# Optimization experiments

Measured on AMD Instinct MI355X. Metric: run time of the kernel, lower is better.

The kernel has to match this reference:

```python
import jax, jax.numpy as jnp
import numpy as np

D_MODEL = 1024
NHEADS = 16
E_HEAD = D_MODEL // NHEADS  # 64
ROPE_BASE = 10000.0


def _rope_cos_sin(L, dim, base, dtype):
    # dim = E_head (even); inv_freq over pairs, GPT-NeoX half-split convention
    inv_freq = 1.0 / (base ** (jnp.arange(0, dim, 2, dtype=jnp.float32) / dim))
    pos = jnp.arange(L, dtype=jnp.float32)
    freqs = pos[:, None] * inv_freq[None, :]  # [L, dim/2]
    return jnp.cos(freqs).astype(dtype), jnp.sin(freqs).astype(dtype)


def _apply_rope(t, cos, sin):
    # t: [B, H, L, Dh]; rotate-half formulation
    d2 = t.shape[-1] // 2
    t1, t2 = t[..., :d2], t[..., d2:]
    return jnp.concatenate([t1 * cos - t2 * sin, t1 * sin + t2 * cos], axis=-1)


def setup_inputs() -> dict:
    key = jax.random.key(0)
    ks = jax.random.split(key, 5)
    B, L = 4, 2048
    x = jax.random.normal(ks[0], (B, L, D_MODEL), dtype=jnp.float32)
    s_in = 1.0 / np.sqrt(D_MODEL)
    W_packed = jax.random.normal(ks[1], (3 * D_MODEL, D_MODEL), dtype=jnp.float32) * s_in
    b_packed = jax.random.normal(ks[2], (3 * D_MODEL,), dtype=jnp.float32) * 0.02
    W_out = jax.random.normal(ks[3], (D_MODEL, D_MODEL), dtype=jnp.float32) * s_in
    b_out = jax.random.normal(ks[4], (D_MODEL,), dtype=jnp.float32) * 0.02
    return {"x": x, "W_packed": W_packed, "b_packed": b_packed, "W_out": W_out, "b_out": b_out}


def reference(x, W_packed, b_packed, W_out, b_out):
    B, L, _ = x.shape
    # 1) packed QKV projection (query is key is value path)
    qkv = jnp.einsum('ble,fe->blf', x, W_packed) + b_packed  # [B, L, 3*D]
    q, k, v = jnp.split(qkv, 3, axis=-1)
    # 2) split heads -> [B, H, L, Dh]
    def heads(t):
        return t.reshape(B, L, NHEADS, E_HEAD).transpose(0, 2, 1, 3)
    q, k, v = heads(q), heads(k), heads(v)
    # 3) RoPE on q, k
    cos, sin = _rope_cos_sin(L, E_HEAD, ROPE_BASE, x.dtype)
    q = _apply_rope(q, cos, sin)
    k = _apply_rope(k, cos, sin)
    # 4) SDPA (non-causal, no dropout)
    scale = 1.0 / np.sqrt(E_HEAD)
    scores = jnp.einsum('bhqd,bhkd->bhqk', q, k) * scale
    attn = jax.nn.softmax(scores, axis=-1)
    out = jnp.einsum('bhqk,bhkd->bhqd', attn, v)
    # 5) merge heads + output projection
    out = out.transpose(0, 2, 1, 3).reshape(B, L, D_MODEL)
    return jnp.einsum('bld,ed->ble', out, W_out) + b_out
```

## Files before the change

kernel.cpp:

```cpp
#include <hip/hip_runtime.h>
#include <hip/hip_bf16.h>
#include <stdint.h>

#define L_SEQ 2048
#define NB    4
#define NH    16
#define EH    64
#define DM    1024
#define MTOT  (NB * L_SEQ)

typedef __attribute__((ext_vector_type(8))) short bf16x8;
typedef __attribute__((ext_vector_type(4))) float f32x4;
typedef __attribute__((ext_vector_type(16))) float f32x16;
typedef __attribute__((ext_vector_type(2))) unsigned uint2v;

static __device__ __forceinline__ float bf2f(short u) {
    union { unsigned int i; float f; } c;
    c.i = ((unsigned int)(unsigned short)u) << 16;
    return c.f;
}
static __device__ __forceinline__ short f2bf(float f) {
    union { float f; unsigned int i; } c; c.f = f;
    unsigned int x = c.i;
    unsigned int r = (x + 0x7fffu + ((x >> 16) & 1u)) >> 16;
    return (short)(unsigned short)r;
}
static __device__ __forceinline__ unsigned cvtpk(float lo, float hi) {
    unsigned r;
    asm volatile("v_cvt_pk_bf16_f32 %0, %1, %2" : "=v"(r) : "v"(lo), "v"(hi));
    return r;
}
static __device__ __forceinline__ float pairmax(float x) {
    union { float f; unsigned u; } c; c.f = x;
    uint2v r = __builtin_amdgcn_permlane32_swap(c.u, c.u, false, false);
    union { unsigned u; float f; } a, b; a.u = r[0]; b.u = r[1];
    return fmaxf(a.f, b.f);
}
static __device__ __forceinline__ float pairsum(float x) {
    union { float f; unsigned u; } c; c.f = x;
    uint2v r = __builtin_amdgcn_permlane32_swap(c.u, c.u, false, false);
    union { unsigned u; float f; } a, b; a.u = r[0]; b.u = r[1];
    return a.f + b.f;
}

static __device__ __forceinline__ void gload_lds16(const void* g, void* lds) {
    __builtin_amdgcn_global_load_lds(
        (const __attribute__((address_space(1))) unsigned int*)g,
        (__attribute__((address_space(3))) unsigned int*)lds, 16, 0, 0);
}

__global__ __launch_bounds__(256) void cvt_k(const float* __restrict__ in,
                                             short* __restrict__ out, int n4) {
    int i = blockIdx.x * 256 + threadIdx.x;
    if (i >= n4) return;
    float4 v = ((const float4*)in)[i];
    short4 o;
    o.x = f2bf(v.x); o.y = f2bf(v.y); o.z = f2bf(v.z); o.w = f2bf(v.w);
    ((short4*)out)[i] = o;
}

__global__ __launch_bounds__(256) void rope_table_k(float* __restrict__ tab) {
    int i = blockIdx.x * 256 + threadIdx.x;
    int l = i >> 5, d = i & 31;
    float inv = powf(10000.0f, -(float)d * (1.0f / 32.0f));
    float fr = (float)l * inv;
    tab[i]         = cosf(fr);
    tab[65536 + i] = sinf(fr);
}

template<int OUTBF16>
__global__ __launch_bounds__(256) void gemm_bt_k(const short* __restrict__ A,
                                                 const short* __restrict__ Bt,
                                                 const float* __restrict__ bias,
                                                 void* __restrict__ Cv,
                                                 int N, int K) {
    __shared__ short As[128 * 64];
    __shared__ short Bs[128 * 64];
    const int t = threadIdx.x;
    const int w = t >> 6, l = t & 63;
    const int wr = w >> 1, wc = w & 1;
    const int lr = l & 15, lh = l >> 4;
    const int m0 = blockIdx.y * 128, n0 = blockIdx.x * 128;
    const int srow = t >> 3;
    const int scol = (t & 7) * 8;

    f32x4 acc[4][4] = {};

    const short* Ab = A + (size_t)(m0 + srow) * K + scol;
    const short* Bb = Bt + (size_t)(n0 + srow) * K + scol;

    for (int k0 = 0; k0 < K; k0 += 64) {
        __syncthreads();
#pragma unroll
        for (int i = 0; i < 4; i++) {
            gload_lds16(Ab + (size_t)(i * 32) * K + k0, As + i * 2048 + w * 512);
            gload_lds16(Bb + (size_t)(i * 32) * K + k0, Bs + i * 2048 + w * 512);
        }
        __syncthreads();
#pragma unroll
        for (int kk = 0; kk < 2; kk++) {
            bf16x8 af[4], bfr[4];
#pragma unroll
            for (int mi = 0; mi < 4; mi++)
                af[mi] = *(const bf16x8*)(As + (wr * 64 + mi * 16 + lr) * 64 + kk * 32 + lh * 8);
#pragma unroll
            for (int nj = 0; nj < 4; nj++)
                bfr[nj] = *(const bf16x8*)(Bs + (wc * 64 + nj * 16 + lr) * 64 + kk * 32 + lh * 8);
            __builtin_amdgcn_s_setprio(1);
#pragma unroll
            for (int mi = 0; mi < 4; mi++)
#pragma unroll
                for (int nj = 0; nj < 4; nj++)
                    acc[mi][nj] = __builtin_amdgcn_mfma_f32_16x16x32_bf16(
                        af[mi], bfr[nj], acc[mi][nj], 0, 0, 0);
            __builtin_amdgcn_s_setprio(0);
        }
    }
#pragma unroll
    for (int mi = 0; mi < 4; mi++) {
#pragma unroll
        for (int nj = 0; nj < 4; nj++) {
            const int row = m0 + wr * 64 + mi * 16 + lh * 4;
            const int col = n0 + wc * 64 + nj * 16 + lr;
            const float bsv = bias[col];
#pragma unroll
            for (int j = 0; j < 4; j++) {
                float v = acc[mi][nj][j] + bsv;
                if (OUTBF16)
                    ((short*)Cv)[(size_t)(row + j) * N + col] = f2bf(v);
                else
                    ((float*)Cv)[(size_t)(row + j) * N + col] = v;
            }
        }
    }
}

__global__ __launch_bounds__(256) void rope_scatter_k(const short* __restrict__ qkv,
                                                      const float* __restrict__ tab,
                                                      short* __restrict__ Q,
                                                      short* __restrict__ Kd) {
    int idx = blockIdx.x * 256 + threadIdx.x;
    int d = idx & 31;
    int h = (idx >> 5) & 15;
    int bl = idx >> 9;
    int l = bl & (L_SEQ - 1);
    int b = bl >> 11;
    float c = tab[l * 32 + d], s = tab[65536 + l * 32 + d];
    const short* row = qkv + (size_t)bl * 3072;
    float q1 = bf2f(row[h * 64 + d]);
    float q2 = bf2f(row[h * 64 + d + 32]);
    float k1 = bf2f(row[1024 + h * 64 + d]);
    float k2 = bf2f(row[1024 + h * 64 + d + 32]);
    size_t ob = ((size_t)((b * 16 + h) * 2048 + l)) * 64;
    const float sc = 0.18033688011112042f;
    Q[ob + d]       = f2bf((q1 * c - q2 * s) * sc);
    Q[ob + d + 32]  = f2bf((q1 * s + q2 * c) * sc);
    int r7 = l & 7;
    int c1 = ((d >> 3) ^ r7) * 8 + (d & 7);
    int c2 = (((d >> 3) | 4) ^ r7) * 8 + (d & 7);
    Kd[ob + c1] = f2bf(k1 * c - k2 * s);
    Kd[ob + c2] = f2bf(k1 * s + k2 * c);
}

__global__ __launch_bounds__(256) void v_trans_k(const short* __restrict__ qkv,
                                                 short* __restrict__ Vt) {
    __shared__ short tile[64 * 65];
    int bh = blockIdx.y;
    int l0 = blockIdx.x * 64;
    int t = threadIdx.x;
    int b = bh >> 4, h = bh & 15;
#pragma unroll
    for (int i = 0; i < 16; i++) {
        int l = i * 4 + (t >> 6);
        int d = t & 63;
        tile[d * 65 + l] = qkv[(size_t)(b * 2048 + l0 + l) * 3072 + 2048 + h * 64 + d];
    }
    __syncthreads();
#pragma unroll
    for (int i = 0; i < 16; i++) {
        int d = i * 4 + (t >> 6);
        int lx = t & 63;
        int cl = (lx & ~0xC) | ((lx & 4) << 1) | ((lx & 8) >> 1);
        int lp = l0 | ((((cl >> 3) ^ (d & 7)) << 3)) | (cl & 7);
        Vt[(size_t)(bh * 64 + d) * 2048 + lp] = tile[d * 65 + lx];
    }
}

__global__ __launch_bounds__(512, 4) void attn_k(const short* __restrict__ Qg,
                                                 const short* __restrict__ Kg,
                                                 const short* __restrict__ Vt,
                                                 short* __restrict__ O) {
    __shared__ short Ks[2][64 * 64];
    __shared__ short Vs[2][64 * 64];
    const int t = threadIdx.x;
    const int w = t >> 6, l = t & 63;
    const int q = l & 31, hi = l >> 5;
    const int r7 = l & 7;

    const int od = blockIdx.x + blockIdx.y * 8;
    const int qblk = (od >> 3) & 7;
    const int bh = (od & 7) * 8 + (od >> 6);
    const int q0 = qblk * 256;

    const short* Qb = Qg + (size_t)bh * (2048 * 64);
    const short* Kb = Kg + (size_t)bh * (2048 * 64);
    const short* Vb = Vt + (size_t)bh * (64 * 2048);

    const int qrow = q0 + w * 32 + q;
    bf16x8 qf[4];
#pragma unroll
    for (int ds = 0; ds < 4; ds++)
        qf[ds] = *(const bf16x8*)(Qb + (size_t)qrow * 64 + ds * 16 + hi * 8);

    f32x16 o0 = {}, o1 = {};
    float m = -1e30f, lsum = 0.0f;

    const int grow = w * 8 + (l >> 3);
    const int gcol = r7 * 8;

    gload_lds16(Kb + (size_t)grow * 64 + gcol, &Ks[0][w * 512]);
    gload_lds16(Vb + (size_t)grow * 2048 + gcol, &Vs[0][w * 512]);
    __syncthreads();

    for (int it = 0; it < 32; ++it) {
        const int cur = it & 1;
        const short* Kc = &Ks[cur][0];
        const short* Vc = &Vs[cur][0];
        if (it < 31) {
            const int kn = (it + 1) * 64;
            gload_lds16(Kb + (size_t)(kn + grow) * 64 + gcol, &Ks[cur ^ 1][w * 512]);
            gload_lds16(Vb + (size_t)grow * 2048 + kn + gcol, &Vs[cur ^ 1][w * 512]);
        }

        f32x16 s0 = {}, s1 = {};
#pragma unroll
        for (int ds = 0; ds < 4; ds++) {
            const int ch = ((ds << 1) | hi) ^ r7;
            bf16x8 k0f = *(const bf16x8*)(Kc + q * 64 + ch * 8);
            bf16x8 k1f = *(const bf16x8*)(Kc + (32 + q) * 64 + ch * 8);
            __builtin_amdgcn_s_setprio(1);
            s0 = __builtin_amdgcn_mfma_f32_32x32x16_bf16(k0f, qf[ds], s0, 0, 0, 0);
            s1 = __builtin_amdgcn_mfma_f32_32x32x16_bf16(k1f, qf[ds], s1, 0, 0, 0);
            __builtin_amdgcn_s_setprio(0);
        }

        float tm[16];
#pragma unroll
        for (int r = 0; r < 16; r++) tm[r] = fmaxf(s0[r], s1[r]);
#pragma unroll
        for (int st = 8; st >= 1; st >>= 1)
#pragma unroll
            for (int i = 0; i < 8; i++) if (i < st) tm[i] = fmaxf(tm[i], tm[i + st]);
        float pm = pairmax(tm[0]);

        if (__any((int)(pm > m + 8.0f))) {
            float mn = fmaxf(m, pm);
            float sc = __builtin_amdgcn_exp2f(m - mn);
            lsum *= sc;
#pragma unroll
            for (int r = 0; r < 16; r++) { o0[r] *= sc; o1[r] *= sc; }
            m = mn;
        }

#pragma unroll
        for (int r = 0; r < 16; r++) {
            s0[r] = __builtin_amdgcn_exp2f(s0[r] - m);
            s1[r] = __builtin_amdgcn_exp2f(s1[r] - m);
        }
        float ts[16];
#pragma unroll
        for (int r = 0; r < 16; r++) ts[r] = s0[r] + s1[r];
#pragma unroll
        for (int st = 8; st >= 1; st >>= 1)
#pragma unroll
            for (int i = 0; i < 8; i++) if (i < st) ts[i] = ts[i] + ts[i + st];
        lsum += pairsum(ts[0]);

        bf16x8 pf[4];
        {
            union { unsigned u[4]; bf16x8 v; } f;
            f.u[0] = cvtpk(s0[0], s0[1]);  f.u[1] = cvtpk(s0[2], s0[3]);
            f.u[2] = cvtpk(s0[4], s0[5]);  f.u[3] = cvtpk(s0[6], s0[7]);
            pf[0] = f.v;
            f.u[0] = cvtpk(s0[8], s0[9]);  f.u[1] = cvtpk(s0[10], s0[11]);
            f.u[2] = cvtpk(s0[12], s0[13]); f.u[3] = cvtpk(s0[14], s0[15]);
            pf[1] = f.v;
            f.u[0] = cvtpk(s1[0], s1[1]);  f.u[1] = cvtpk(s1[2], s1[3]);
            f.u[2] = cvtpk(s1[4], s1[5]);  f.u[3] = cvtpk(s1[6], s1[7]);
            pf[2] = f.v;
            f.u[0] = cvtpk(s1[8], s1[9]);  f.u[1] = cvtpk(s1[10], s1[11]);
            f.u[2] = cvtpk(s1[12], s1[13]); f.u[3] = cvtpk(s1[14], s1[15]);
            pf[3] = f.v;
        }

#pragma unroll
        for (int ks = 0; ks < 4; ks++) {
            const int ch = ((ks << 1) | hi) ^ r7;
            bf16x8 v0f = *(const bf16x8*)(Vc + q * 64 + ch * 8);
            bf16x8 v1f = *(const bf16x8*)(Vc + (32 + q) * 64 + ch * 8);
            __builtin_amdgcn_s_setprio(1);
            o0 = __builtin_amdgcn_mfma_f32_32x32x16_bf16(v0f, pf[ks], o0, 0, 0, 0);
            o1 = __builtin_amdgcn_mfma_f32_32x32x16_bf16(v1f, pf[ks], o1, 0, 0, 0);
            __builtin_amdgcn_s_setprio(0);
        }

        __syncthreads();
    }

    const float inv = 1.0f / lsum;
    const int b = bh >> 4, h = bh & 15;
    short* Orow = O + (size_t)(b * 2048 + qrow) * 1024 + h * 64;
#pragma unroll
    for (int g = 0; g < 4; g++) {
        unsigned w0 = cvtpk(o0[g * 4 + 0] * inv, o0[g * 4 + 1] * inv);
        unsigned w1 = cvtpk(o0[g * 4 + 2] * inv, o0[g * 4 + 3] * inv);
        unsigned long long p0 = (unsigned long long)w0 | ((unsigned long long)w1 << 32);
        *(unsigned long long*)(Orow + g * 8 + hi * 4) = p0;
        unsigned w2 = cvtpk(o1[g * 4 + 0] * inv, o1[g * 4 + 1] * inv);
        unsigned w3 = cvtpk(o1[g * 4 + 2] * inv, o1[g * 4 + 3] * inv);
        unsigned long long p1 = (unsigned long long)w2 | ((unsigned long long)w3 << 32);
        *(unsigned long long*)(Orow + 32 + g * 8 + hi * 4) = p1;
    }
}

extern "C" void kernel_launch(void* const* d_in, const int* in_sizes, int n_in,
                              void* d_out, int out_size, void* d_ws, size_t ws_size,
                              hipStream_t stream) {
    const float* x  = (const float*)d_in[0];
    const float* Wp = (const float*)d_in[1];
    const float* bp = (const float*)d_in[2];
    const float* Wo = (const float*)d_in[3];
    const float* bo = (const float*)d_in[4];

    char* ws = (char*)d_ws;
    const size_t SZ_XB  = (size_t)MTOT * DM * 2;
    const size_t SZ_WPB = (size_t)3 * DM * DM * 2;
    const size_t SZ_WOB = (size_t)DM * DM * 2;
    const size_t SZ_QKV = (size_t)MTOT * 3 * DM * 2;
    const size_t SZ_BHLE = (size_t)MTOT * DM * 2;

    short* xb   = (short*)(ws);
    short* wpb  = (short*)(ws + SZ_XB);
    short* wob  = (short*)(ws + SZ_XB + SZ_WPB);
    short* qkvb = (short*)(ws + SZ_XB + SZ_WPB + SZ_WOB);
    short* Qb   = (short*)(ws + SZ_XB + SZ_WPB + SZ_WOB + SZ_QKV);
    short* Kb   = (short*)(ws + SZ_XB + SZ_WPB + SZ_WOB + SZ_QKV + SZ_BHLE);
    short* Vtb  = (short*)(ws + SZ_XB + SZ_WPB + SZ_WOB + SZ_QKV + 2 * SZ_BHLE);
    short* Ob   = (short*)(ws + SZ_XB + SZ_WPB + SZ_WOB + SZ_QKV + 3 * SZ_BHLE);
    float* tab  = (float*)(ws + SZ_XB + SZ_WPB + SZ_WOB + SZ_QKV + 4 * SZ_BHLE);

    cvt_k<<<8192, 256, 0, stream>>>(x, xb, MTOT * DM / 4);
    cvt_k<<<3072, 256, 0, stream>>>(Wp, wpb, 3 * DM * DM / 4);
    cvt_k<<<1024, 256, 0, stream>>>(Wo, wob, DM * DM / 4);
    rope_table_k<<<256, 256, 0, stream>>>(tab);

    gemm_bt_k<1><<<dim3(24, 64), 256, 0, stream>>>(xb, wpb, bp, qkvb, 3 * DM, DM);

    rope_scatter_k<<<16384, 256, 0, stream>>>(qkvb, tab, Qb, Kb);
    v_trans_k<<<dim3(32, 64), 256, 0, stream>>>(qkvb, Vtb);

    attn_k<<<dim3(8, 64), 512, 0, stream>>>(Qb, Kb, Vtb, Ob);

    gemm_bt_k<0><<<dim3(8, 64), 256, 0, stream>>>(Ob, wob, bo, d_out, DM, DM);
}
```

Before: 220.3 us.

## Fuse RoPE and V transpose into QKV GEMM epilogue, merge casts, MFMA row sums

The QKV GEMM now applies bias, RoPE and scaling itself and writes Q, swizzled K and transposed V straight from its accumulators. This removes the bf16 qkv intermediate and the separate rope_scatter and v_trans kernels. The three fp32-to-bf16 conversion launches are merged into one kernel. In attention, the softmax row sum comes from an extra MFMA against a ones vector instead of shuffle reductions, which adds MFMA work but removes VALU reductions. The new epilogue uses scattered 2-byte stores and per-element table lookups, which may be less coalesced than before.

```diff
diff --git a/kernel.cpp b/kernel.cpp
--- a/kernel.cpp
+++ b/kernel.cpp
@@ -36,12 +36,6 @@
     union { unsigned u; float f; } a, b; a.u = r[0]; b.u = r[1];
     return fmaxf(a.f, b.f);
 }
-static __device__ __forceinline__ float pairsum(float x) {
-    union { float f; unsigned u; } c; c.f = x;
-    uint2v r = __builtin_amdgcn_permlane32_swap(c.u, c.u, false, false);
-    union { unsigned u; float f; } a, b; a.u = r[0]; b.u = r[1];
-    return a.f + b.f;
-}
 
 static __device__ __forceinline__ void gload_lds16(const void* g, void* lds) {
     __builtin_amdgcn_global_load_lds(
@@ -49,14 +43,21 @@
         (__attribute__((address_space(3))) unsigned int*)lds, 16, 0, 0);
 }
 
-__global__ __launch_bounds__(256) void cvt_k(const float* __restrict__ in,
-                                             short* __restrict__ out, int n4) {
-    int i = blockIdx.x * 256 + threadIdx.x;
-    if (i >= n4) return;
-    float4 v = ((const float4*)in)[i];
+__global__ __launch_bounds__(256) void cvt3_k(const float* __restrict__ x,
+                                              const float* __restrict__ wp,
+                                              const float* __restrict__ wo,
+                                              short* __restrict__ xb,
+                                              short* __restrict__ wpb,
+                                              short* __restrict__ wob) {
+    int bid = blockIdx.x;
+    const float* src; short* dst; int i;
+    if (bid < 8192)       { src = x;  dst = xb;  i = bid * 256 + threadIdx.x; }
+    else if (bid < 11264) { src = wp; dst = wpb; i = (bid - 8192) * 256 + threadIdx.x; }
+    else                  { src = wo; dst = wob; i = (bid - 11264) * 256 + threadIdx.x; }
+    float4 v = ((const float4*)src)[i];
     short4 o;
     o.x = f2bf(v.x); o.y = f2bf(v.y); o.z = f2bf(v.z); o.w = f2bf(v.w);
-    ((short4*)out)[i] = o;
+    ((short4*)dst)[i] = o;
 }
 
 __global__ __launch_bounds__(256) void rope_table_k(float* __restrict__ tab) {
@@ -68,12 +69,13 @@
     tab[65536 + i] = sinf(fr);
 }
 
-template<int OUTBF16>
-__global__ __launch_bounds__(256) void gemm_bt_k(const short* __restrict__ A,
-                                                 const short* __restrict__ Bt,
-                                                 const float* __restrict__ bias,
-                                                 void* __restrict__ Cv,
-                                                 int N, int K) {
+__global__ __launch_bounds__(256) void qkv_gemm_k(const short* __restrict__ A,
+                                                  const short* __restrict__ Bt,
+                                                  const float* __restrict__ bias,
+                                                  const float* __restrict__ tab,
+                                                  short* __restrict__ Q,
+                                                  short* __restrict__ Kd,
+                                                  short* __restrict__ Vt) {
     __shared__ short As[128 * 64];
     __shared__ short Bs[128 * 64];
     const int t = threadIdx.x;
@@ -86,15 +88,15 @@
 
     f32x4 acc[4][4] = {};
 
-    const short* Ab = A + (size_t)(m0 + srow) * K + scol;
-    const short* Bb = Bt + (size_t)(n0 + srow) * K + scol;
-
-    for (int k0 = 0; k0 < K; k0 += 64) {
+    const short* Ab = A + (size_t)(m0 + srow) * 1024 + scol;
+    const short* Bb = Bt + (size_t)(n0 + srow) * 1024 + scol;
+
+    for (int k0 = 0; k0 < 1024; k0 += 64) {
         __syncthreads();
 #pragma unroll
         for (int i = 0; i < 4; i++) {
-            gload_lds16(Ab + (size_t)(i * 32) * K + k0, As + i * 2048 + w * 512);
-            gload_lds16(Bb + (size_t)(i * 32) * K + k0, Bs + i * 2048 + w * 512);
+            gload_lds16(Ab + (size_t)(i * 32) * 1024 + k0, As + i * 2048 + w * 512);
+            gload_lds16(Bb + (size_t)(i * 32) * 1024 + k0, Bs + i * 2048 + w * 512);
         }
         __syncthreads();
 #pragma unroll
@@ -116,6 +118,108 @@
             __builtin_amdgcn_s_setprio(0);
         }
     }
+
+    const int part = n0 >> 10;
+    const int h = ((n0 & 1023) >> 6) + wc;
+    const float sc = 0.18033688011112042f;
+
+    if (part == 2) {
+#pragma unroll
+        for (int mi = 0; mi < 4; mi++) {
+            const int rowb = m0 + wr * 64 + mi * 16 + lh * 4;
+            const int b = rowb >> 11;
+            const int lbase = (rowb & 2047) & ~63;
+            const int lp = (((mi * 2 + (lh & 1)) ^ (lr & 7)) << 3) | ((lh >> 1) * 4);
+#pragma unroll
+            for (int nj = 0; nj < 4; nj++) {
+                const int dv = nj * 16 + lr;
+                const float bv = bias[n0 + wc * 64 + nj * 16 + lr];
+                short4 sv;
+                sv.x = f2bf(acc[mi][nj][0] + bv);
+                sv.y = f2bf(acc[mi][nj][1] + bv);
+                sv.z = f2bf(acc[mi][nj][2] + bv);
+                sv.w = f2bf(acc[mi][nj][3] + bv);
+                *(short4*)(Vt + (size_t)((b * 16 + h) * 64 + dv) * 2048 + lbase + lp) = sv;
+            }
+        }
+    } else {
+#pragma unroll
+        for (int mi = 0; mi < 4; mi++) {
+            const int rowb = m0 + wr * 64 + mi * 16 + lh * 4;
+#pragma unroll
+            for (int njl = 0; njl < 2; njl++) {
+                const int d2 = njl * 16 + lr;
+                const float b1 = bias[n0 + wc * 64 + njl * 16 + lr];
+                const float b2 = bias[n0 + wc * 64 + (njl + 2) * 16 + lr];
+#pragma unroll
+                for (int j = 0; j < 4; j++) {
+                    const int rr = rowb + j;
+                    const int ll = rr & 2047, b = rr >> 11;
+                    const float c = tab[ll * 32 + d2], s = tab[65536 + ll * 32 + d2];
+                    const float t1 = acc[mi][njl][j] + b1;
+                    const float t2 = acc[mi][njl + 2][j] + b2;
+                    const size_t ob = ((size_t)((b * 16 + h) * 2048 + ll)) * 64;
+                    if (part == 0) {
+                        Q[ob + d2]      = f2bf((t1 * c - t2 * s) * sc);
+                        Q[ob + d2 + 32] = f2bf((t1 * s + t2 * c) * sc);
+                    } else {
+                        const int r7l = ll & 7;
+                        Kd[ob + (((d2 >> 3) ^ r7l) * 8) + (d2 & 7)]         = f2bf(t1 * c - t2 * s);
+                        Kd[ob + ((((d2 >> 3) | 4) ^ r7l) * 8) + (d2 & 7)]   = f2bf(t1 * s + t2 * c);
+                    }
+                }
+            }
+        }
+    }
+}
+
+__global__ __launch_bounds__(256) void gemm_out_k(const short* __restrict__ A,
+                                                  const short* __restrict__ Bt,
+                                                  const float* __restrict__ bias,
+                                                  float* __restrict__ Cv,
+                                                  int N, int K) {
+    __shared__ short As[128 * 64];
+    __shared__ short Bs[128 * 64];
+    const int t = threadIdx.x;
+    const int w = t >> 6, l = t & 63;
+    const int wr = w >> 1, wc = w & 1;
+    const int lr = l & 15, lh = l >> 4;
+    const int m0 = blockIdx.y * 128, n0 = blockIdx.x * 128;
+    const int srow = t >> 3;
+    const int scol = (t & 7) * 8;
+
+    f32x4 acc[4][4] = {};
+
+    const short* Ab = A + (size_t)(m0 + srow) * K + scol;
+    const short* Bb = Bt + (size_t)(n0 + srow) * K + scol;
+
+    for (int k0 = 0; k0 < K; k0 += 64) {
+        __syncthreads();
+#pragma unroll
+        for (int i = 0; i < 4; i++) {
+            gload_lds16(Ab + (size_t)(i * 32) * K + k0, As + i * 2048 + w * 512);
+            gload_lds16(Bb + (size_t)(i * 32) * K + k0, Bs + i * 2048 + w * 512);
+        }
+        __syncthreads();
+#pragma unroll
+        for (int kk = 0; kk < 2; kk++) {
+            bf16x8 af[4], bfr[4];
+#pragma unroll
+            for (int mi = 0; mi < 4; mi++)
+                af[mi] = *(const bf16x8*)(As + (wr * 64 + mi * 16 + lr) * 64 + kk * 32 + lh * 8);
+#pragma unroll
+            for (int nj = 0; nj < 4; nj++)
+                bfr[nj] = *(const bf16x8*)(Bs + (wc * 64 + nj * 16 + lr) * 64 + kk * 32 + lh * 8);
+            __builtin_amdgcn_s_setprio(1);
+#pragma unroll
+            for (int mi = 0; mi < 4; mi++)
+#pragma unroll
+                for (int nj = 0; nj < 4; nj++)
+                    acc[mi][nj] = __builtin_amdgcn_mfma_f32_16x16x32_bf16(
+                        af[mi], bfr[nj], acc[mi][nj], 0, 0, 0);
+            __builtin_amdgcn_s_setprio(0);
+        }
+    }
 #pragma unroll
     for (int mi = 0; mi < 4; mi++) {
 #pragma unroll
@@ -124,65 +228,9 @@
             const int col = n0 + wc * 64 + nj * 16 + lr;
             const float bsv = bias[col];
 #pragma unroll
-            for (int j = 0; j < 4; j++) {
-                float v = acc[mi][nj][j] + bsv;
-                if (OUTBF16)
-                    ((short*)Cv)[(size_t)(row + j) * N + col] = f2bf(v);
-                else
-                    ((float*)Cv)[(size_t)(row + j) * N + col] = v;
-            }
-        }
-    }
-}
-
-__global__ __launch_bounds__(256) void rope_scatter_k(const short* __restrict__ qkv,
-                                                      const float* __restrict__ tab,
-                                                      short* __restrict__ Q,
-                                                      short* __restrict__ Kd) {
-    int idx = blockIdx.x * 256 + threadIdx.x;
-    int d = idx & 31;
-    int h = (idx >> 5) & 15;
-    int bl = idx >> 9;
-    int l = bl & (L_SEQ - 1);
-    int b = bl >> 11;
-    float c = tab[l * 32 + d], s = tab[65536 + l * 32 + d];
-    const short* row = qkv + (size_t)bl * 3072;
-    float q1 = bf2f(row[h * 64 + d]);
-    float q2 = bf2f(row[h * 64 + d + 32]);
-    float k1 = bf2f(row[1024 + h * 64 + d]);
-    float k2 = bf2f(row[1024 + h * 64 + d + 32]);
-    size_t ob = ((size_t)((b * 16 + h) * 2048 + l)) * 64;
-    const float sc = 0.18033688011112042f;
-    Q[ob + d]       = f2bf((q1 * c - q2 * s) * sc);
-    Q[ob + d + 32]  = f2bf((q1 * s + q2 * c) * sc);
-    int r7 = l & 7;
-    int c1 = ((d >> 3) ^ r7) * 8 + (d & 7);
-    int c2 = (((d >> 3) | 4) ^ r7) * 8 + (d & 7);
-    Kd[ob + c1] = f2bf(k1 * c - k2 * s);
-    Kd[ob + c2] = f2bf(k1 * s + k2 * c);
-}
-
-__global__ __launch_bounds__(256) void v_trans_k(const short* __restrict__ qkv,
-                                                 short* __restrict__ Vt) {
-    __shared__ short tile[64 * 65];
-    int bh = blockIdx.y;
-    int l0 = blockIdx.x * 64;
-    int t = threadIdx.x;
-    int b = bh >> 4, h = bh & 15;
-#pragma unroll
-    for (int i = 0; i < 16; i++) {
-        int l = i * 4 + (t >> 6);
-        int d = t & 63;
-        tile[d * 65 + l] = qkv[(size_t)(b * 2048 + l0 + l) * 3072 + 2048 + h * 64 + d];
-    }
-    __syncthreads();
-#pragma unroll
-    for (int i = 0; i < 16; i++) {
-        int d = i * 4 + (t >> 6);
-        int lx = t & 63;
-        int cl = (lx & ~0xC) | ((lx & 4) << 1) | ((lx & 8) >> 1);
-        int lp = l0 | ((((cl >> 3) ^ (d & 7)) << 3)) | (cl & 7);
-        Vt[(size_t)(bh * 64 + d) * 2048 + lp] = tile[d * 65 + lx];
+            for (int j = 0; j < 4; j++)
+                Cv[(size_t)(row + j) * N + col] = acc[mi][nj][j] + bsv;
+        }
     }
 }
 
@@ -212,8 +260,11 @@
     for (int ds = 0; ds < 4; ds++)
         qf[ds] = *(const bf16x8*)(Qb + (size_t)qrow * 64 + ds * 16 + hi * 8);
 
-    f32x16 o0 = {}, o1 = {};
-    float m = -1e30f, lsum = 0.0f;
+    const short one_bf = (short)0x3F80;
+    const bf16x8 ones = {one_bf, one_bf, one_bf, one_bf, one_bf, one_bf, one_bf, one_bf};
+
+    f32x16 o0 = {}, o1 = {}, os = {};
+    float m = -1e30f;
 
     const int grow = w * 8 + (l >> 3);
     const int gcol = r7 * 8;
@@ -244,21 +295,19 @@
             __builtin_amdgcn_s_setprio(0);
         }
 
-        float tm[16];
-#pragma unroll
-        for (int r = 0; r < 16; r++) tm[r] = fmaxf(s0[r], s1[r]);
-#pragma unroll
-        for (int st = 8; st >= 1; st >>= 1)
-#pragma unroll
-            for (int i = 0; i < 8; i++) if (i < st) tm[i] = fmaxf(tm[i], tm[i + st]);
-        float pm = pairmax(tm[0]);
+        float a[8];
+#pragma unroll
+        for (int i = 0; i < 8; i++)
+            a[i] = fmaxf(fmaxf(s0[i], s0[i + 8]), fmaxf(s1[i], s1[i + 8]));
+        float pm = pairmax(fmaxf(
+            fmaxf(fmaxf(a[0], a[1]), fmaxf(a[2], a[3])),
+            fmaxf(fmaxf(a[4], a[5]), fmaxf(a[6], a[7]))));
 
         if (__any((int)(pm > m + 8.0f))) {
             float mn = fmaxf(m, pm);
             float sc = __builtin_amdgcn_exp2f(m - mn);
-            lsum *= sc;
-#pragma unroll
-            for (int r = 0; r < 16; r++) { o0[r] *= sc; o1[r] *= sc; }
+#pragma unroll
+            for (int r = 0; r < 16; r++) { o0[r] *= sc; o1[r] *= sc; os[r] *= sc; }
             m = mn;
         }
 
@@ -267,14 +316,6 @@
             s0[r] = __builtin_amdgcn_exp2f(s0[r] - m);
             s1[r] = __builtin_amdgcn_exp2f(s1[r] - m);
         }
-        float ts[16];
-#pragma unroll
-        for (int r = 0; r < 16; r++) ts[r] = s0[r] + s1[r];
-#pragma unroll
-        for (int st = 8; st >= 1; st >>= 1)
-#pragma unroll
-            for (int i = 0; i < 8; i++) if (i < st) ts[i] = ts[i] + ts[i + st];
-        lsum += pairsum(ts[0]);
 
         bf16x8 pf[4];
         {
@@ -301,13 +342,14 @@
             __builtin_amdgcn_s_setprio(1);
             o0 = __builtin_amdgcn_mfma_f32_32x32x16_bf16(v0f, pf[ks], o0, 0, 0, 0);
             o1 = __builtin_amdgcn_mfma_f32_32x32x16_bf16(v1f, pf[ks], o1, 0, 0, 0);
+            os = __builtin_amdgcn_mfma_f32_32x32x16_bf16(ones, pf[ks], os, 0, 0, 0);
             __builtin_amdgcn_s_setprio(0);
         }
 
         __syncthreads();
     }
 
-    const float inv = 1.0f / lsum;
+    const float inv = 1.0f / os[0];
     const int b = bh >> 4, h = bh & 15;
     short* Orow = O + (size_t)(b * 2048 + qrow) * 1024 + h * 64;
 #pragma unroll
@@ -336,30 +378,23 @@
     const size_t SZ_XB  = (size_t)MTOT * DM * 2;
     const size_t SZ_WPB = (size_t)3 * DM * DM * 2;
     const size_t SZ_WOB = (size_t)DM * DM * 2;
-    const size_t SZ_QKV = (size_t)MTOT * 3 * DM * 2;
     const size_t SZ_BHLE = (size_t)MTOT * DM * 2;
 
     short* xb   = (short*)(ws);
     short* wpb  = (short*)(ws + SZ_XB);
     short* wob  = (short*)(ws + SZ_XB + SZ_WPB);
-    short* qkvb = (short*)(ws + SZ_XB + SZ_WPB + SZ_WOB);
-    short* Qb   = (short*)(ws + SZ_XB + SZ_WPB + SZ_WOB + SZ_QKV);
-    short* Kb   = (short*)(ws + SZ_XB + SZ_WPB + SZ_WOB + SZ_QKV + SZ_BHLE);
-    short* Vtb  = (short*)(ws + SZ_XB + SZ_WPB + SZ_WOB + SZ_QKV + 2 * SZ_BHLE);
-    short* Ob   = (short*)(ws + SZ_XB + SZ_WPB + SZ_WOB + SZ_QKV + 3 * SZ_BHLE);
-    float* tab  = (float*)(ws + SZ_XB + SZ_WPB + SZ_WOB + SZ_QKV + 4 * SZ_BHLE);
-
-    cvt_k<<<8192, 256, 0, stream>>>(x, xb, MTOT * DM / 4);
-    cvt_k<<<3072, 256, 0, stream>>>(Wp, wpb, 3 * DM * DM / 4);
-    cvt_k<<<1024, 256, 0, stream>>>(Wo, wob, DM * DM / 4);
+    short* Qb   = (short*)(ws + SZ_XB + SZ_WPB + SZ_WOB);
+    short* Kb   = (short*)(ws + SZ_XB + SZ_WPB + SZ_WOB + SZ_BHLE);
+    short* Vtb  = (short*)(ws + SZ_XB + SZ_WPB + SZ_WOB + 2 * SZ_BHLE);
+    short* Ob   = (short*)(ws + SZ_XB + SZ_WPB + SZ_WOB + 3 * SZ_BHLE);
+    float* tab  = (float*)(ws + SZ_XB + SZ_WPB + SZ_WOB + 4 * SZ_BHLE);
+
+    cvt3_k<<<12288, 256, 0, stream>>>(x, Wp, Wo, xb, wpb, wob);
     rope_table_k<<<256, 256, 0, stream>>>(tab);
 
-    gemm_bt_k<1><<<dim3(24, 64), 256, 0, stream>>>(xb, wpb, bp, qkvb, 3 * DM, DM);
-
-    rope_scatter_k<<<16384, 256, 0, stream>>>(qkvb, tab, Qb, Kb);
-    v_trans_k<<<dim3(32, 64), 256, 0, stream>>>(qkvb, Vtb);
+    qkv_gemm_k<<<dim3(24, 64), 256, 0, stream>>>(xb, wpb, bp, tab, Qb, Kb, Vtb);
 
     attn_k<<<dim3(8, 64), 512, 0, stream>>>(Qb, Kb, Vtb, Ob);
 
-    gemm_bt_k<0><<<dim3(8, 64), 256, 0, stream>>>(Ob, wob, bo, d_out, DM, DM);
-}
+    gemm_out_k<<<dim3(8, 64), 256, 0, stream>>>(Ob, wob, bo, (float*)d_out, DM, DM);
+}
```

Result: slower. 229.0 us (+4.0%).

## Use 256x256 double-buffered GEMM, fuse conversions, compute softmax sum via MFMA

Applied to the files above, without the earlier changes.

Replaces the 128x128 single-buffered GEMM with a 512-thread 256x256 tile kernel that uses two-stage LDS prefetch, a swizzled LDS layout and block-index swizzling. The three fp32-to-bf16 conversion launches become one kernel. In attention, the softmax denominator is accumulated by an extra MFMA against a ones vector instead of VALU reductions and lane swaps, and the max reduction is flattened. Larger tiles raise data reuse but yield only 128 blocks for the output projection, which may underfill the GPU; the extra MFMA adds matrix-core work.

```diff
diff --git a/kernel.cpp b/kernel.cpp
--- a/kernel.cpp
+++ b/kernel.cpp
@@ -36,12 +36,6 @@
     union { unsigned u; float f; } a, b; a.u = r[0]; b.u = r[1];
     return fmaxf(a.f, b.f);
 }
-static __device__ __forceinline__ float pairsum(float x) {
-    union { float f; unsigned u; } c; c.f = x;
-    uint2v r = __builtin_amdgcn_permlane32_swap(c.u, c.u, false, false);
-    union { unsigned u; float f; } a, b; a.u = r[0]; b.u = r[1];
-    return a.f + b.f;
-}
 
 static __device__ __forceinline__ void gload_lds16(const void* g, void* lds) {
     __builtin_amdgcn_global_load_lds(
@@ -49,14 +43,21 @@
         (__attribute__((address_space(3))) unsigned int*)lds, 16, 0, 0);
 }
 
-__global__ __launch_bounds__(256) void cvt_k(const float* __restrict__ in,
-                                             short* __restrict__ out, int n4) {
-    int i = blockIdx.x * 256 + threadIdx.x;
-    if (i >= n4) return;
-    float4 v = ((const float4*)in)[i];
+__global__ __launch_bounds__(256) void cvt3_k(const float* __restrict__ x,
+                                              const float* __restrict__ wp,
+                                              const float* __restrict__ wo,
+                                              short* __restrict__ xb,
+                                              short* __restrict__ wpb,
+                                              short* __restrict__ wob) {
+    int bid = blockIdx.x;
+    const float* src; short* dst; int i;
+    if (bid < 8192)       { src = x;  dst = xb;  i = bid * 256 + threadIdx.x; }
+    else if (bid < 11264) { src = wp; dst = wpb; i = (bid - 8192) * 256 + threadIdx.x; }
+    else                  { src = wo; dst = wob; i = (bid - 11264) * 256 + threadIdx.x; }
+    float4 v = ((const float4*)src)[i];
     short4 o;
     o.x = f2bf(v.x); o.y = f2bf(v.y); o.z = f2bf(v.z); o.w = f2bf(v.w);
-    ((short4*)out)[i] = o;
+    ((short4*)dst)[i] = o;
 }
 
 __global__ __launch_bounds__(256) void rope_table_k(float* __restrict__ tab) {
@@ -68,63 +69,91 @@
     tab[65536 + i] = sinf(fr);
 }
 
-template<int OUTBF16>
-__global__ __launch_bounds__(256) void gemm_bt_k(const short* __restrict__ A,
-                                                 const short* __restrict__ Bt,
-                                                 const float* __restrict__ bias,
-                                                 void* __restrict__ Cv,
-                                                 int N, int K) {
-    __shared__ short As[128 * 64];
-    __shared__ short Bs[128 * 64];
+template<int OUTBF16, int NBX>
+__global__ __launch_bounds__(512, 2) void gemm256_k(const short* __restrict__ A,
+                                                    const short* __restrict__ Bt,
+                                                    const float* __restrict__ bias,
+                                                    void* __restrict__ Cv) {
+    __shared__ short lds[2][2][256 * 32];
     const int t = threadIdx.x;
     const int w = t >> 6, l = t & 63;
-    const int wr = w >> 1, wc = w & 1;
+    const int wm = w >> 2, wn = w & 3;
     const int lr = l & 15, lh = l >> 4;
-    const int m0 = blockIdx.y * 128, n0 = blockIdx.x * 128;
-    const int srow = t >> 3;
-    const int scol = (t & 7) * 8;
-
-    f32x4 acc[4][4] = {};
-
-    const short* Ab = A + (size_t)(m0 + srow) * K + scol;
-    const short* Bb = Bt + (size_t)(n0 + srow) * K + scol;
-
-    for (int k0 = 0; k0 < K; k0 += 64) {
-        __syncthreads();
-#pragma unroll
-        for (int i = 0; i < 4; i++) {
-            gload_lds16(Ab + (size_t)(i * 32) * K + k0, As + i * 2048 + w * 512);
-            gload_lds16(Bb + (size_t)(i * 32) * K + k0, Bs + i * 2048 + w * 512);
-        }
-        __syncthreads();
-#pragma unroll
-        for (int kk = 0; kk < 2; kk++) {
-            bf16x8 af[4], bfr[4];
-#pragma unroll
-            for (int mi = 0; mi < 4; mi++)
-                af[mi] = *(const bf16x8*)(As + (wr * 64 + mi * 16 + lr) * 64 + kk * 32 + lh * 8);
-#pragma unroll
-            for (int nj = 0; nj < 4; nj++)
-                bfr[nj] = *(const bf16x8*)(Bs + (wc * 64 + nj * 16 + lr) * 64 + kk * 32 + lh * 8);
-            __builtin_amdgcn_s_setprio(1);
-#pragma unroll
-            for (int mi = 0; mi < 4; mi++)
-#pragma unroll
-                for (int nj = 0; nj < 4; nj++)
-                    acc[mi][nj] = __builtin_amdgcn_mfma_f32_16x16x32_bf16(
-                        af[mi], bfr[nj], acc[mi][nj], 0, 0, 0);
-            __builtin_amdgcn_s_setprio(0);
-        }
-    }
-#pragma unroll
-    for (int mi = 0; mi < 4; mi++) {
-#pragma unroll
-        for (int nj = 0; nj < 4; nj++) {
-            const int row = m0 + wr * 64 + mi * 16 + lh * 4;
-            const int col = n0 + wc * 64 + nj * 16 + lr;
+    const int N = NBX * 256;
+
+    const int nblk = NBX * 32;
+    int fid = blockIdx.x + blockIdx.y * NBX;
+    int swz = (fid & 7) * (nblk >> 3) + (fid >> 3);
+    const int n0 = (swz % NBX) * 256;
+    const int m0 = (swz / NBX) * 256;
+
+    const int lrow = l >> 2;
+    const int schunk = (l & 3) ^ ((l >> 3) & 3);
+
+    const short* Ag = A + (size_t)(m0 + lrow) * 1024 + schunk * 8;
+    const short* Bg = Bt + (size_t)(n0 + lrow) * 1024 + schunk * 8;
+
+    auto STAGE = [&](int kt, int buf) {
+#pragma unroll
+        for (int j = 0; j < 2; ++j) {
+            const int r = (w * 2 + j) * 16;
+            gload_lds16(Ag + (size_t)r * 1024 + kt * 32, &lds[buf][0][r * 32]);
+            gload_lds16(Bg + (size_t)r * 1024 + kt * 32, &lds[buf][1][r * 32]);
+        }
+    };
+
+    f32x4 acc[8][4] = {};
+
+    STAGE(0, 0);
+    STAGE(1, 1);
+    asm volatile("s_waitcnt vmcnt(4)" ::: "memory");
+    __builtin_amdgcn_s_barrier();
+
+    const int fch = (lh ^ ((lr >> 1) & 3)) << 3;
+
+#pragma unroll 2
+    for (int kt = 0; kt < 32; ++kt) {
+        const int c = kt & 1;
+        const short* Al = &lds[c][0][0];
+        const short* Bl = &lds[c][1][0];
+
+        bf16x8 bfr[4], af[8];
+#pragma unroll
+        for (int nj = 0; nj < 4; ++nj)
+            bfr[nj] = *(const bf16x8*)(Bl + (wn * 64 + nj * 16 + lr) * 32 + fch);
+#pragma unroll
+        for (int mi = 0; mi < 8; ++mi)
+            af[mi] = *(const bf16x8*)(Al + (wm * 128 + mi * 16 + lr) * 32 + fch);
+
+        __builtin_amdgcn_s_setprio(1);
+#pragma unroll
+        for (int mi = 0; mi < 8; ++mi)
+#pragma unroll
+            for (int nj = 0; nj < 4; ++nj)
+                acc[mi][nj] = __builtin_amdgcn_mfma_f32_16x16x32_bf16(
+                    af[mi], bfr[nj], acc[mi][nj], 0, 0, 0);
+        __builtin_amdgcn_s_setprio(0);
+
+        asm volatile("s_waitcnt lgkmcnt(0)" ::: "memory");
+        __builtin_amdgcn_s_barrier();
+        if (kt + 2 < 32) {
+            STAGE(kt + 2, c);
+            asm volatile("s_waitcnt vmcnt(4)" ::: "memory");
+        } else {
+            asm volatile("s_waitcnt vmcnt(0)" ::: "memory");
+        }
+        __builtin_amdgcn_s_barrier();
+    }
+
+#pragma unroll
+    for (int mi = 0; mi < 8; ++mi) {
+#pragma unroll
+        for (int nj = 0; nj < 4; ++nj) {
+            const int row = m0 + wm * 128 + mi * 16 + lh * 4;
+            const int col = n0 + wn * 64 + nj * 16 + lr;
             const float bsv = bias[col];
 #pragma unroll
-            for (int j = 0; j < 4; j++) {
+            for (int j = 0; j < 4; ++j) {
                 float v = acc[mi][nj][j] + bsv;
                 if (OUTBF16)
                     ((short*)Cv)[(size_t)(row + j) * N + col] = f2bf(v);
@@ -212,8 +241,11 @@
     for (int ds = 0; ds < 4; ds++)
         qf[ds] = *(const bf16x8*)(Qb + (size_t)qrow * 64 + ds * 16 + hi * 8);
 
-    f32x16 o0 = {}, o1 = {};
-    float m = -1e30f, lsum = 0.0f;
+    const short one_bf = (short)0x3F80;
+    const bf16x8 ones = {one_bf, one_bf, one_bf, one_bf, one_bf, one_bf, one_bf, one_bf};
+
+    f32x16 o0 = {}, o1 = {}, os = {};
+    float m = -1e30f;
 
     const int grow = w * 8 + (l >> 3);
     const int gcol = r7 * 8;
@@ -244,21 +276,19 @@
             __builtin_amdgcn_s_setprio(0);
         }
 
-        float tm[16];
-#pragma unroll
-        for (int r = 0; r < 16; r++) tm[r] = fmaxf(s0[r], s1[r]);
-#pragma unroll
-        for (int st = 8; st >= 1; st >>= 1)
-#pragma unroll
-            for (int i = 0; i < 8; i++) if (i < st) tm[i] = fmaxf(tm[i], tm[i + st]);
-        float pm = pairmax(tm[0]);
+        float a[8];
+#pragma unroll
+        for (int i = 0; i < 8; i++)
+            a[i] = fmaxf(fmaxf(s0[i], s0[i + 8]), fmaxf(s1[i], s1[i + 8]));
+        float pm = pairmax(fmaxf(
+            fmaxf(fmaxf(a[0], a[1]), fmaxf(a[2], a[3])),
+            fmaxf(fmaxf(a[4], a[5]), fmaxf(a[6], a[7]))));
 
         if (__any((int)(pm > m + 8.0f))) {
             float mn = fmaxf(m, pm);
             float sc = __builtin_amdgcn_exp2f(m - mn);
-            lsum *= sc;
-#pragma unroll
-            for (int r = 0; r < 16; r++) { o0[r] *= sc; o1[r] *= sc; }
+#pragma unroll
+            for (int r = 0; r < 16; r++) { o0[r] *= sc; o1[r] *= sc; os[r] *= sc; }
             m = mn;
         }
 
@@ -267,14 +297,6 @@
             s0[r] = __builtin_amdgcn_exp2f(s0[r] - m);
             s1[r] = __builtin_amdgcn_exp2f(s1[r] - m);
         }
-        float ts[16];
-#pragma unroll
-        for (int r = 0; r < 16; r++) ts[r] = s0[r] + s1[r];
-#pragma unroll
-        for (int st = 8; st >= 1; st >>= 1)
-#pragma unroll
-            for (int i = 0; i < 8; i++) if (i < st) ts[i] = ts[i] + ts[i + st];
-        lsum += pairsum(ts[0]);
 
         bf16x8 pf[4];
         {
@@ -301,13 +323,14 @@
             __builtin_amdgcn_s_setprio(1);
             o0 = __builtin_amdgcn_mfma_f32_32x32x16_bf16(v0f, pf[ks], o0, 0, 0, 0);
             o1 = __builtin_amdgcn_mfma_f32_32x32x16_bf16(v1f, pf[ks], o1, 0, 0, 0);
+            os = __builtin_amdgcn_mfma_f32_32x32x16_bf16(ones, pf[ks], os, 0, 0, 0);
             __builtin_amdgcn_s_setprio(0);
         }
 
         __syncthreads();
     }
 
-    const float inv = 1.0f / lsum;
+    const float inv = 1.0f / os[0];
     const int b = bh >> 4, h = bh & 15;
     short* Orow = O + (size_t)(b * 2048 + qrow) * 1024 + h * 64;
 #pragma unroll
@@ -349,17 +372,15 @@
     short* Ob   = (short*)(ws + SZ_XB + SZ_WPB + SZ_WOB + SZ_QKV + 3 * SZ_BHLE);
     float* tab  = (float*)(ws + SZ_XB + SZ_WPB + SZ_WOB + SZ_QKV + 4 * SZ_BHLE);
 
-    cvt_k<<<8192, 256, 0, stream>>>(x, xb, MTOT * DM / 4);
-    cvt_k<<<3072, 256, 0, stream>>>(Wp, wpb, 3 * DM * DM / 4);
-    cvt_k<<<1024, 256, 0, stream>>>(Wo, wob, DM * DM / 4);
+    cvt3_k<<<12288, 256, 0, stream>>>(x, Wp, Wo, xb, wpb, wob);
     rope_table_k<<<256, 256, 0, stream>>>(tab);
 
-    gemm_bt_k<1><<<dim3(24, 64), 256, 0, stream>>>(xb, wpb, bp, qkvb, 3 * DM, DM);
+    gemm256_k<1, 12><<<dim3(12, 32), 512, 0, stream>>>(xb, wpb, bp, qkvb);
 
     rope_scatter_k<<<16384, 256, 0, stream>>>(qkvb, tab, Qb, Kb);
     v_trans_k<<<dim3(32, 64), 256, 0, stream>>>(qkvb, Vtb);
 
     attn_k<<<dim3(8, 64), 512, 0, stream>>>(Qb, Kb, Vtb, Ob);
 
-    gemm_bt_k<0><<<dim3(8, 64), 256, 0, stream>>>(Ob, wob, bo, d_out, DM, DM);
-}
+    gemm256_k<0, 4><<<dim3(4, 32), 512, 0, stream>>>(Ob, wob, bo, d_out);
+}
```

Result: no change. 220.7 us (+0.2%).
